# Kernel tuning notes

Hardware: AMD Instinct MI355X
Metric: run time of the kernel (lower is better)

The kernel has to match this reference:

```python
import jax, jax.numpy as jnp
import numpy as np

D_MODEL, D_INNER, D_STATE, NHEADS, HEADDIM, D_CONV, CHUNK = 1024, 2048, 128, 32, 64, 4, 64
B_SZ, L = 2, 2048
EPS = 1e-5


def _segsum_exp(x):
    # x: (..., T) -> exp of lower-triangular cumulative segment sums, (..., T, T)
    cs = jnp.cumsum(x, axis=-1)
    seg = cs[..., :, None] - cs[..., None, :]
    T = x.shape[-1]
    mask = jnp.tril(jnp.ones((T, T), dtype=bool))
    return jnp.exp(jnp.where(mask, seg, 0.0)) * mask


def ssd(x, A, B, C, chunk):
    # x: (b,l,h,p), A: (b,l,h), B,C: (b,l,n)
    b, l, h, p = x.shape
    n = B.shape[-1]
    c = l // chunk
    x = x.reshape(b, c, chunk, h, p)
    A = A.reshape(b, c, chunk, h).transpose(0, 3, 1, 2)        # (b,h,c,s)
    B = B.reshape(b, c, chunk, n)
    C = C.reshape(b, c, chunk, n)
    A_cum = jnp.cumsum(A, axis=-1)                              # (b,h,c,s)
    Lmat = _segsum_exp(A)                                       # (b,h,c,s,s)
    # intra-chunk (diagonal block) output
    Y_diag = jnp.einsum('bcln,bcsn,bhcls,bcshp->bclhp', C, B, Lmat, x)
    # per-chunk final states
    decay_states = jnp.exp(A_cum[..., -1:] - A_cum)             # (b,h,c,s)
    states = jnp.einsum('bcsn,bhcs,bcshp->bchpn', B, decay_states, x)
    states = jnp.concatenate([jnp.zeros_like(states[:, :1]), states], axis=1)  # (b,c+1,h,p,n)
    # inter-chunk recurrence over chunk sums
    chunk_sums = jnp.pad(A_cum[..., -1], ((0, 0), (0, 0), (1, 0)))  # (b,h,c+1)
    decay_chunk = _segsum_exp(chunk_sums)                       # (b,h,c+1,c+1)
    new_states = jnp.einsum('bhzc,bchpn->bzhpn', decay_chunk, states)
    states_in, final_state = new_states[:, :-1], new_states[:, -1]
    out_decay = jnp.exp(A_cum)                                  # (b,h,c,s)
    Y_off = jnp.einsum('bcln,bchpn,bhcl->bclhp', C, states_in, out_decay)
    Y = (Y_diag + Y_off).reshape(b, l, h, p)
    return Y, final_state


def causal_depthwise_conv(x, w, b):
    # x: (B, C, L), w: (C, K), b: (C,)
    K = w.shape[-1]
    Llen = x.shape[-1]
    xp = jnp.pad(x, ((0, 0), (0, 0), (K - 1, 0)))
    out = b[None, :, None]
    for k in range(K):
        out = out + w[None, :, k, None] * xp[:, :, k:k + Llen]
    return out


def setup_inputs() -> dict:
    key = jax.random.key(0)
    ks = jax.random.split(key, 9)
    d_in_proj = 2 * D_INNER + 2 * D_STATE + NHEADS
    conv_dim = D_INNER + 2 * D_STATE
    return {
        'u': jax.random.normal(ks[0], (B_SZ, L, D_MODEL), jnp.float32),
        'W_in': jax.random.normal(ks[1], (d_in_proj, D_MODEL), jnp.float32) * (D_MODEL ** -0.5),
        'conv_w': jax.random.normal(ks[2], (conv_dim, D_CONV), jnp.float32) * (D_CONV ** -0.5),
        'conv_b': jax.random.normal(ks[3], (conv_dim,), jnp.float32) * 0.01,
        'dt_bias': jax.random.normal(ks[4], (NHEADS,), jnp.float32),
        'A_log': jnp.log(1.0 + 15.0 * jax.random.uniform(ks[5], (NHEADS,), jnp.float32)),
        'D': jax.random.normal(ks[6], (NHEADS,), jnp.float32),
        'norm_w': jnp.ones((D_INNER,), jnp.float32),
        'W_out': jax.random.normal(ks[8], (D_MODEL, D_INNER), jnp.float32) * (D_INNER ** -0.5),
    }


def reference(u, W_in, conv_w, conv_b, dt_bias, A_log, D, norm_w, W_out):
    zxbcdt = u @ W_in.T                                        # (B,L,d_in_proj)
    z = zxbcdt[..., :D_INNER]
    xBC = zxbcdt[..., D_INNER:2 * D_INNER + 2 * D_STATE]
    dt = jax.nn.softplus(zxbcdt[..., -NHEADS:] + dt_bias)      # (B,L,H)
    # causal depthwise conv + silu
    xBC = causal_depthwise_conv(xBC.transpose(0, 2, 1), conv_w, conv_b).transpose(0, 2, 1)
    xBC = jax.nn.silu(xBC)
    A = -jnp.exp(A_log)                                        # (H,)
    x = xBC[..., :D_INNER].reshape(u.shape[0], u.shape[1], NHEADS, HEADDIM)
    Bm = xBC[..., D_INNER:D_INNER + D_STATE]
    Cm = xBC[..., D_INNER + D_STATE:]
    y, _ = ssd(x * dt[..., None], A * dt, Bm, Cm, CHUNK)
    y = y + x * D[:, None]
    y = y.reshape(u.shape[0], u.shape[1], D_INNER)
    # gated RMSNorm
    y = y * jax.nn.silu(z)
    y = y * jax.lax.rsqrt(jnp.mean(y * y, axis=-1, keepdims=True) + EPS) * norm_w
    return y @ W_out.T
```

## Files before the change

### kernel.cpp

```cpp
#include <hip/hip_runtime.h>
#include <hip/hip_bf16.h>
#include <math.h>

#define D_MODEL 1024
#define D_INNER 2048
#define D_STATE 128
#define NHEADS 32
#define HEADDIM 64
#define CHUNK 64
#define B_SZ 2
#define LSEQ 2048
#define BL (B_SZ*LSEQ)
#define DPROJ (2*D_INNER + 2*D_STATE + NHEADS)
#define CONV_DIM (D_INNER + 2*D_STATE)
#define NCHUNK (LSEQ/CHUNK)
#define NPAD1 4480
#define EPSF 1e-5f

typedef __attribute__((ext_vector_type(8))) _Float16 half8;
typedef __attribute__((ext_vector_type(4))) _Float16 half4;
typedef __attribute__((ext_vector_type(4))) float f32x4;

__device__ __forceinline__ float siluf(float v){ return v / (1.0f + expf(-v)); }
__device__ __forceinline__ float softplusf(float v){ return v > 20.0f ? v : log1pf(expf(v)); }
__device__ __forceinline__ unsigned short f2h(float x){
  union { _Float16 h; unsigned short u; } v; v.h = (_Float16)x;
  return v.u;
}
__device__ __forceinline__ float h2f(unsigned short x){
  union { unsigned short u; _Float16 h; } v; v.u = x;
  return (float)v.h;
}
__device__ __forceinline__ _Float16 h2h(unsigned short x){
  union { unsigned short u; _Float16 h; } v; v.u = x;
  return v.h;
}

typedef const __attribute__((address_space(1))) void gvoid_t;
typedef __attribute__((address_space(3))) void lvoid_t;
__device__ __forceinline__ void gl_lds16(const void* gsrc, void* ldst) {
  gvoid_t* g = reinterpret_cast<gvoid_t*>((uintptr_t)gsrc);
  lvoid_t* l = reinterpret_cast<lvoid_t*>((unsigned int)(uintptr_t)ldst);
  __builtin_amdgcn_global_load_lds(g, l, 16, 0, 0);
}

#define NU4  (BL*D_MODEL/4)
#define NW4  (NPAD1*D_MODEL/4)
#define NWo4 (D_MODEL*D_INNER/4)
#define NCVT (NU4+NW4+NWo4)

__global__ void cvt_all(const float* __restrict__ u, const float* __restrict__ W_in,
                        const float* __restrict__ W_out, const float* __restrict__ norm_w,
                        unsigned short* __restrict__ u_h, unsigned short* __restrict__ Win_h,
                        unsigned short* __restrict__ Wg_h) {
  int i = blockIdx.x*256 + threadIdx.x;
  if (i >= NCVT) return;
  if (i < NU4) {
    float4 v = *(const float4*)(u + (size_t)i*4);
    ushort4 o; o.x=f2h(v.x); o.y=f2h(v.y); o.z=f2h(v.z); o.w=f2h(v.w);
    *(ushort4*)(u_h + (size_t)i*4) = o;
  } else if (i < NU4 + NW4) {
    int q = i - NU4;
    int row = q / (D_MODEL/4);
    ushort4 o; o.x=0; o.y=0; o.z=0; o.w=0;
    if (row < DPROJ) {
      float4 v = *(const float4*)(W_in + (size_t)q*4);
      o.x=f2h(v.x); o.y=f2h(v.y); o.z=f2h(v.z); o.w=f2h(v.w);
    }
    *(ushort4*)(Win_h + (size_t)q*4) = o;
  } else {
    int q = i - NU4 - NW4;
    int colq = q % (D_INNER/4);
    float4 v = *(const float4*)(W_out + (size_t)q*4);
    float4 g = *(const float4*)(norm_w + (size_t)colq*4);
    ushort4 o; o.x=f2h(v.x*g.x); o.y=f2h(v.y*g.y); o.z=f2h(v.z*g.z); o.w=f2h(v.w*g.w);
    *(ushort4*)(Wg_h + (size_t)q*4) = o;
  }
}

template<int OUT_F16>
__global__ __launch_bounds__(256) void gemm_f16_pipe(const unsigned short* __restrict__ A,
    const unsigned short* __restrict__ W, void* __restrict__ Cv,
    const float* __restrict__ Sc, int N, int K) {
  __shared__ unsigned short lds[4*2*4096];
  const int t   = threadIdx.x;
  const int wid = t >> 6, l = t & 63;
  const int gx = gridDim.x, gy = gridDim.y;
  int bid = blockIdx.y * gx + blockIdx.x;
  int k   = bid & 7;
  int j   = bid >> 3;
  int rpx = gy >> 3;
  int r   = j % rpx;
  int colIdx = j / rpx;
  int row = k*rpx + r;
  int col = (colIdx + k*(gx >> 3)) % gx;
  const int m0 = row * 128;
  const int n0 = col * 128;
  const int wr = wid >> 1, wc = wid & 1;
  const int fr = l & 15, cg = l >> 4;
  const int NT = K >> 5;

  int srow[2]; int scol[2];
  #pragma unroll
  for (int i=0;i<2;++i){
    int s = i*256 + t;
    int rr = s >> 2, c = s & 3;
    int sw = (rr + (rr>>2)) & 3;
    srow[i] = rr; scol[i] = (c ^ sw) * 8;
  }
  const unsigned short* Abase = A + (size_t)m0 * K;
  const unsigned short* Wbase = W + (size_t)n0 * K;

#define STAGE(tt, slot) { \
    int kk = (tt) << 5; \
    unsigned short* La = &lds[(slot)*8192]; \
    unsigned short* Lb = &lds[(slot)*8192 + 4096]; \
    gl_lds16(Abase + (size_t)srow[0]*K + kk + scol[0], (char*)La + (0*256+t)*16); \
    gl_lds16(Abase + (size_t)srow[1]*K + kk + scol[1], (char*)La + (1*256+t)*16); \
    gl_lds16(Wbase + (size_t)srow[0]*K + kk + scol[0], (char*)Lb + (0*256+t)*16); \
    gl_lds16(Wbase + (size_t)srow[1]*K + kk + scol[1], (char*)Lb + (1*256+t)*16); \
  }

#define COMPUTE(slot) { \
    const unsigned short* La = &lds[(slot)*8192]; \
    const unsigned short* Lb = &lds[(slot)*8192 + 4096]; \
    half8 af[4], bfv[4]; \
    _Pragma("unroll") \
    for (int m=0;m<4;++m){ \
      int rr = wr*64 + m*16 + fr; \
      int sw = (rr + (rr>>2)) & 3; \
      af[m] = *(const half8*)&La[(rr*4 + (cg ^ sw))*8]; \
    } \
    _Pragma("unroll") \
    for (int n=0;n<4;++n){ \
      int rr = wc*64 + n*16 + fr; \
      int sw = (rr + (rr>>2)) & 3; \
      bfv[n] = *(const half8*)&Lb[(rr*4 + (cg ^ sw))*8]; \
    } \
    __builtin_amdgcn_s_setprio(1); \
    _Pragma("unroll") \
    for (int m=0;m<4;++m) \
      _Pragma("unroll") \
      for (int n=0;n<4;++n) \
        acc[m][n] = __builtin_amdgcn_mfma_f32_16x16x32_f16(af[m], bfv[n], acc[m][n], 0, 0, 0); \
    __builtin_amdgcn_s_setprio(0); \
  }

  f32x4 acc[4][4] = {};
  STAGE(0, 0);
  STAGE(1, 1);
  STAGE(2, 2);
  STAGE(3, 3);

  for (int tt = 0; tt < NT; tt += 2) {
    if (tt + 4 < NT) { asm volatile("s_waitcnt vmcnt(8)" ::: "memory"); }
    else             { asm volatile("s_waitcnt vmcnt(0)" ::: "memory"); }
    __builtin_amdgcn_s_barrier();
    asm volatile("" ::: "memory");

    COMPUTE(tt & 3);
    COMPUTE((tt + 1) & 3);

    asm volatile("s_waitcnt lgkmcnt(0)" ::: "memory");
    __builtin_amdgcn_s_barrier();
    asm volatile("" ::: "memory");
    if (tt + 4 < NT) {
      STAGE(tt + 4, (tt + 4) & 3);
      if (tt + 5 < NT) STAGE(tt + 5, (tt + 5) & 3);
    }
  }
#undef COMPUTE
#undef STAGE

  const int crow = m0 + wr*64 + (l >> 4) * 4;
  const int ccol0 = n0 + wc*64 + fr;
  #pragma unroll
  for (int m = 0; m < 4; ++m) {
    #pragma unroll
    for (int n = 0; n < 4; ++n) {
      int colo = ccol0 + n*16;
      if (colo < N) {
        if (OUT_F16) {
          unsigned short* cp = (unsigned short*)Cv + (size_t)(crow + m*16)*N + colo;
          #pragma unroll
          for (int jj = 0; jj < 4; ++jj) cp[(size_t)jj*N] = f2h(acc[m][n][jj]);
        } else {
          float* cp = (float*)Cv + (size_t)(crow + m*16)*N + colo;
          #pragma unroll
          for (int jj = 0; jj < 4; ++jj) cp[(size_t)jj*N] = acc[m][n][jj] * Sc[crow + m*16 + jj];
        }
      }
    }
  }
}

__global__ __launch_bounds__(256) void gemm_f16_64(const unsigned short* __restrict__ A,
    const unsigned short* __restrict__ W, float* __restrict__ C,
    const float* __restrict__ Sc, int N, int K) {
  __shared__ unsigned short lds[4*6144];
  const int t   = threadIdx.x;
  const int wid = t >> 6, l = t & 63;
  const int gx = gridDim.x, gy = gridDim.y;
  int bid = blockIdx.y * gx + blockIdx.x;
  int k   = bid & 7;
  int j   = bid >> 3;
  int rpx = gy >> 3;
  int r   = j % rpx;
  int colIdx = j / rpx;
  const int m0 = (k*rpx + r) * 64;
  const int n0 = ((colIdx + k*(gx >> 3)) % gx) * 128;
  const int fr = l & 15, cg = l >> 4;
  const int NT = K >> 5;

  const int srw  = t >> 2;
  const int sw_  = (srw + (srw>>2)) & 3;
  const int scl  = ((t & 3) ^ sw_) * 8;
  const unsigned short* Abase = A + (size_t)m0 * K;
  const unsigned short* Wbase = W + (size_t)n0 * K;

#define STG64(tt, slot) { \
    int kk = (tt) << 5; \
    char* Ls = (char*)lds + (slot)*12288; \
    gl_lds16(Abase + (size_t)srw*K + kk + scl,        Ls + t*16); \
    gl_lds16(Wbase + (size_t)srw*K + kk + scl,        Ls + 4096 + t*16); \
    gl_lds16(Wbase + (size_t)(64+srw)*K + kk + scl,   Ls + 4096 + (256+t)*16); \
  }

#define CMP64(slot) { \
    const unsigned short* La = &lds[(slot)*6144]; \
    const unsigned short* Lb = &lds[(slot)*6144 + 2048]; \
    half8 af[4], bfv[2]; \
    _Pragma("unroll") \
    for (int m=0;m<4;++m){ \
      int rr = m*16 + fr; \
      int sw = (rr + (rr>>2)) & 3; \
      af[m] = *(const half8*)&La[(rr*4 + (cg ^ sw))*8]; \
    } \
    _Pragma("unroll") \
    for (int n=0;n<2;++n){ \
      int rr = wid*32 + n*16 + fr; \
      int sw = (rr + (rr>>2)) & 3; \
      bfv[n] = *(const half8*)&Lb[(rr*4 + (cg ^ sw))*8]; \
    } \
    __builtin_amdgcn_s_setprio(1); \
    _Pragma("unroll") \
    for (int m=0;m<4;++m) \
      _Pragma("unroll") \
      for (int n=0;n<2;++n) \
        acc[m][n] = __builtin_amdgcn_mfma_f32_16x16x32_f16(af[m], bfv[n], acc[m][n], 0, 0, 0); \
    __builtin_amdgcn_s_setprio(0); \
  }

  f32x4 acc[4][2] = {};
  STG64(0, 0);
  STG64(1, 1);
  STG64(2, 2);
  STG64(3, 3);

  for (int tt = 0; tt < NT; tt += 2) {
    if (tt + 4 < NT) { asm volatile("s_waitcnt vmcnt(6)" ::: "memory"); }
    else             { asm volatile("s_waitcnt vmcnt(0)" ::: "memory"); }
    __builtin_amdgcn_s_barrier();
    asm volatile("" ::: "memory");

    CMP64(tt & 3);
    CMP64((tt + 1) & 3);

    asm volatile("s_waitcnt lgkmcnt(0)" ::: "memory");
    __builtin_amdgcn_s_barrier();
    asm volatile("" ::: "memory");
    if (tt + 4 < NT) {
      STG64(tt + 4, (tt + 4) & 3);
      if (tt + 5 < NT) STG64(tt + 5, (tt + 5) & 3);
    }
  }
#undef CMP64
#undef STG64

  const int crow = m0 + cg * 4;
  const int ccol0 = n0 + wid*32 + fr;
  #pragma unroll
  for (int m = 0; m < 4; ++m) {
    #pragma unroll
    for (int n = 0; n < 2; ++n) {
      int colo = ccol0 + n*16;
      float* cp = C + (size_t)(crow + m*16)*N + colo;
      #pragma unroll
      for (int jj = 0; jj < 4; ++jj) cp[(size_t)jj*N] = acc[m][n][jj] * Sc[crow + m*16 + jj];
    }
  }
}

__global__ __launch_bounds__(64) void dtacum_kernel(const unsigned short* __restrict__ zx,
    const float* __restrict__ dt_bias, const float* __restrict__ A_log,
    float* __restrict__ dt, float* __restrict__ A_cum) {
  int blk = blockIdx.x;
  int c = blk & 31, h = (blk >> 5) & 31, b = blk >> 10;
  int l = threadIdx.x;
  int row = b*LSEQ + c*CHUNK + l;
  float v = h2f(zx[(size_t)row*DPROJ + (2*D_INNER + 2*D_STATE) + h]) + dt_bias[h];
  float dtv = softplusf(v);
  dt[row*NHEADS + h] = dtv;
  float val = -expf(A_log[h]) * dtv;
  #pragma unroll
  for (int off = 1; off < 64; off <<= 1) {
    float nv = __shfl_up(val, off, 64);
    if (l >= off) val += nv;
  }
  A_cum[blk*64 + l] = val;
}

__global__ __launch_bounds__(256) void conv8_kernel(const unsigned short* __restrict__ zx,
    const float* __restrict__ w, const float* __restrict__ bias, unsigned short* __restrict__ xBC) {
  int idx = blockIdx.x*256 + threadIdx.x;
  if (idx >= (BL/8)*(CONV_DIM/4)) return;
  int c4  = idx % (CONV_DIM/4);
  int rb  = idx / (CONV_DIM/4);
  int ch  = c4 * 4;
  int row0 = rb * 8;
  int l0   = row0 & (LSEQ-1);
  float4 r[11];
  #pragma unroll
  for (int jj=0;jj<11;++jj){
    int li = l0 + jj - 3;
    if (li >= 0) {
      ushort4 v = *(const ushort4*)&zx[(size_t)(row0 + jj - 3)*DPROJ + D_INNER + ch];
      r[jj] = make_float4(h2f(v.x), h2f(v.y), h2f(v.z), h2f(v.w));
    } else r[jj] = make_float4(0.f,0.f,0.f,0.f);
  }
  float4 wv[4];
  #pragma unroll
  for (int c=0;c<4;++c) wv[c] = *(const float4*)&w[(ch+c)*4];
  float4 bv = *(const float4*)&bias[ch];
  #pragma unroll
  for (int j=0;j<8;++j){
    float4 acc = bv;
    acc.x += wv[0].x*r[j].x + wv[0].y*r[j+1].x + wv[0].z*r[j+2].x + wv[0].w*r[j+3].x;
    acc.y += wv[1].x*r[j].y + wv[1].y*r[j+1].y + wv[1].z*r[j+2].y + wv[1].w*r[j+3].y;
    acc.z += wv[2].x*r[j].z + wv[2].y*r[j+1].z + wv[2].z*r[j+2].z + wv[2].w*r[j+3].z;
    acc.w += wv[3].x*r[j].w + wv[3].y*r[j+1].w + wv[3].z*r[j+2].w + wv[3].w*r[j+3].w;
    ushort4 o; o.x=f2h(siluf(acc.x)); o.y=f2h(siluf(acc.y)); o.z=f2h(siluf(acc.z)); o.w=f2h(siluf(acc.w));
    *(ushort4*)&xBC[(size_t)(row0+j)*CONV_DIM + ch] = o;
  }
}

__global__ __launch_bounds__(256) void g_kernel(const unsigned short* __restrict__ xBC,
                                                unsigned short* __restrict__ G) {
  int blk = blockIdx.x >> 2;
  int lq  = blockIdx.x & 3;
  int b = blk >> 5, c = blk & 31;
  __shared__ float Bsh[64][129];
  int t = threadIdx.x;
  int row0 = b*LSEQ + c*CHUNK;
  #pragma unroll
  for (int j=0;j<8;++j){
    int e0 = (j*256 + t)*4;
    int s = e0 >> 7, n = e0 & 127;
    ushort4 v = *(const ushort4*)&xBC[(size_t)(row0+s)*CONV_DIM + D_INNER + n];
    Bsh[s][n+0] = h2f(v.x); Bsh[s][n+1] = h2f(v.y);
    Bsh[s][n+2] = h2f(v.z); Bsh[s][n+3] = h2f(v.w);
  }
  __syncthreads();
  int l = lq*16 + (t >> 4), s0 = (t & 15) * 4;
  const unsigned short* Cp = &xBC[(size_t)(row0+l)*CONV_DIM + D_INNER + D_STATE];
  float acc[4] = {};
  #pragma unroll 4
  for (int n4=0;n4<32;++n4){
    ushort4 cv4 = *(const ushort4*)&Cp[n4*4];
    float cv[4] = { h2f(cv4.x), h2f(cv4.y), h2f(cv4.z), h2f(cv4.w) };
    #pragma unroll
    for (int kk=0;kk<4;++kk){
      #pragma unroll
      for (int j=0;j<4;++j) acc[j] += cv[kk] * Bsh[s0+j][n4*4+kk];
    }
  }
  unsigned short* Gp = &G[(size_t)blk*4096 + l*64 + s0];
  ushort4 o; o.x=f2h(acc[0]); o.y=f2h(acc[1]); o.z=f2h(acc[2]); o.w=f2h(acc[3]);
  *(ushort4*)Gp = o;
}

__global__ __launch_bounds__(256) void states_mfma(const unsigned short* __restrict__ xBC,
    const float* __restrict__ dt, const float* __restrict__ A_cum, unsigned short* __restrict__ states) {
  int blk = blockIdx.x;
  int h = blk & 31, c = (blk>>5)&31, b = blk>>10;
  __shared__ _Float16 Bt[128][72];
  __shared__ _Float16 xdT[64][72];
  __shared__ float Ac[64], dtl[64];
  int t = threadIdx.x;
  int wid = t >> 6, ln = t & 63;
  int row0 = b*LSEQ + c*CHUNK;
  if (t < 64){ Ac[t] = A_cum[((b*32+h)*32 + c)*64 + t]; dtl[t] = dt[(row0+t)*NHEADS + h]; }
  __syncthreads();
  float AcL = Ac[63];
  #pragma unroll
  for (int j=0;j<8;++j){
    int e0 = (j*256+t)*4;
    int s = e0 >> 7, n = e0 & 127;
    ushort4 v = *(const ushort4*)&xBC[(size_t)(row0+s)*CONV_DIM + D_INNER + n];
    Bt[n+0][s] = h2h(v.x); Bt[n+1][s] = h2h(v.y);
    Bt[n+2][s] = h2h(v.z); Bt[n+3][s] = h2h(v.w);
  }
  #pragma unroll
  for (int j=0;j<4;++j){
    int e0 = (j*256+t)*4;
    int s = e0 >> 6, p = e0 & 63;
    float sc = dtl[s] * expf(AcL - Ac[s]);
    ushort4 v = *(const ushort4*)&xBC[(size_t)(row0+s)*CONV_DIM + h*HEADDIM + p];
    xdT[p+0][s] = (_Float16)(h2f(v.x)*sc);
    xdT[p+1][s] = (_Float16)(h2f(v.y)*sc);
    xdT[p+2][s] = (_Float16)(h2f(v.z)*sc);
    xdT[p+3][s] = (_Float16)(h2f(v.w)*sc);
  }
  __syncthreads();
  const int fr = ln & 15, fk = (ln >> 4) * 8;
  f32x4 acc[4][2] = {};
  #pragma unroll
  for (int ks = 0; ks < 2; ++ks){
    half8 a[4], bb[2];
    #pragma unroll
    for (int pt=0;pt<4;++pt) a[pt] = *(const half8*)&xdT[pt*16+fr][ks*32+fk];
    #pragma unroll
    for (int nt=0;nt<2;++nt) bb[nt] = *(const half8*)&Bt[(wid*2+nt)*16+fr][ks*32+fk];
    #pragma unroll
    for (int pt=0;pt<4;++pt)
      #pragma unroll
      for (int nt=0;nt<2;++nt)
        acc[pt][nt] = __builtin_amdgcn_mfma_f32_16x16x32_f16(a[pt], bb[nt], acc[pt][nt], 0, 0, 0);
  }
  unsigned short* Sp = &states[(size_t)blk*8192];
  #pragma unroll
  for (int pt=0;pt<4;++pt){
    int p0 = pt*16 + (ln>>4)*4;
    #pragma unroll
    for (int nt=0;nt<2;++nt){
      int n = (wid*2+nt)*16 + fr;
      #pragma unroll
      for (int j=0;j<4;++j) Sp[(p0+j)*128 + n] = f2h(acc[pt][nt][j]);
    }
  }
}

__global__ __launch_bounds__(256) void scan_kernel(const float* __restrict__ A_cum,
                                                   unsigned short* __restrict__ states) {
  int g  = blockIdx.x & 7;
  int bh = blockIdx.x >> 3;
  int b = bh >> 5, h = bh & 31;
  int t = threadIdx.x;
  int off = g*1024 + t*4;
  ushort4 tmp[NCHUNK];
  float dec[NCHUNK];
  #pragma unroll
  for (int c=0;c<NCHUNK;++c){
    tmp[c] = *(const ushort4*)&states[(size_t)((b*32+c)*32 + h)*8192 + off];
    dec[c] = A_cum[((b*32+h)*32 + c)*64 + 63];
  }
  float s0=0.f, s1=0.f, s2=0.f, s3=0.f;
  #pragma unroll
  for (int c=0;c<NCHUNK;++c){
    float d = expf(dec[c]);
    ushort4 o; o.x=f2h(s0); o.y=f2h(s1); o.z=f2h(s2); o.w=f2h(s3);
    *(ushort4*)&states[(size_t)((b*32+c)*32 + h)*8192 + off] = o;
    s0 = s0*d + h2f(tmp[c].x);
    s1 = s1*d + h2f(tmp[c].y);
    s2 = s2*d + h2f(tmp[c].z);
    s3 = s3*d + h2f(tmp[c].w);
  }
}

__global__ __launch_bounds__(256) void y_mfma(const unsigned short* __restrict__ xBC,
    const unsigned short* __restrict__ zx, const float* __restrict__ dt,
    const float* __restrict__ A_cum, const unsigned short* __restrict__ G,
    const unsigned short* __restrict__ states, const float* __restrict__ Dp,
    unsigned short* __restrict__ y_pre) {
  int blk = blockIdx.x;
  int h = blk & 31, c = (blk>>5)&31, b = blk>>10;
  __shared__ _Float16 Cl[64][136];
  __shared__ _Float16 Sin[64][136];
  __shared__ _Float16 Ms[64][72];
  __shared__ _Float16 xdT[64][72];
  __shared__ float Ac[64], dtl[64];
  int t = threadIdx.x;
  int wid = t >> 6, ln = t & 63;
  int row0 = b*LSEQ + c*CHUNK;
  if (t < 64){ Ac[t] = A_cum[((b*32+h)*32 + c)*64 + t]; dtl[t] = dt[(row0+t)*NHEADS + h]; }
  __syncthreads();
  #pragma unroll
  for (int j=0;j<8;++j){
    int e0 = (j*256+t)*4; int l = e0>>7, n = e0&127;
    float sc = expf(Ac[l]);
    ushort4 v = *(const ushort4*)&xBC[(size_t)(row0+l)*CONV_DIM + D_INNER + D_STATE + n];
    half4 hv = { (_Float16)(h2f(v.x)*sc), (_Float16)(h2f(v.y)*sc),
                 (_Float16)(h2f(v.z)*sc), (_Float16)(h2f(v.w)*sc) };
    *(half4*)&Cl[l][n] = hv;
  }
  {
    const unsigned short* Sg = &states[(size_t)blk*8192];
    #pragma unroll
    for (int j=0;j<8;++j){
      int elem = (j*256+t)*4; int p = elem>>7, n = elem&127;
      ushort4 v = *(const ushort4*)&Sg[elem];
      half4 hv = { h2h(v.x), h2h(v.y), h2h(v.z), h2h(v.w) };
      *(half4*)&Sin[p][n] = hv;
    }
  }
  #pragma unroll
  for (int j=0;j<4;++j){
    int e0 = (j*256+t)*4; int s = e0>>6, p = e0&63;
    float sc = dtl[s];
    ushort4 v = *(const ushort4*)&xBC[(size_t)(row0+s)*CONV_DIM + h*HEADDIM + p];
    xdT[p+0][s] = (_Float16)(h2f(v.x)*sc);
    xdT[p+1][s] = (_Float16)(h2f(v.y)*sc);
    xdT[p+2][s] = (_Float16)(h2f(v.z)*sc);
    xdT[p+3][s] = (_Float16)(h2f(v.w)*sc);
  }
  {
    const unsigned short* Gp = &G[(size_t)(b*32+c)*4096];
    #pragma unroll
    for (int j=0;j<4;++j){
      int e0 = (j*256+t)*4; int l = e0>>6, s = e0&63;
      ushort4 gv = *(const ushort4*)&Gp[e0];
      float al = Ac[l];
      Ms[l][s+0] = (s+0 <= l) ? (_Float16)(h2f(gv.x) * expf(al-Ac[s+0])) : (_Float16)0.f;
      Ms[l][s+1] = (s+1 <= l) ? (_Float16)(h2f(gv.y) * expf(al-Ac[s+1])) : (_Float16)0.f;
      Ms[l][s+2] = (s+2 <= l) ? (_Float16)(h2f(gv.z) * expf(al-Ac[s+2])) : (_Float16)0.f;
      Ms[l][s+3] = (s+3 <= l) ? (_Float16)(h2f(gv.w) * expf(al-Ac[s+3])) : (_Float16)0.f;
    }
  }
  __syncthreads();
  const int wr = wid >> 1, wc = wid & 1;
  const int fr = ln & 15, fk = (ln >> 4) * 8;
  f32x4 acc[2][2] = {};
  #pragma unroll
  for (int ks = 0; ks < 4; ++ks){
    half8 a[2], bb[2];
    #pragma unroll
    for (int lt=0;lt<2;++lt) a[lt] = *(const half8*)&Cl[(wr*2+lt)*16+fr][ks*32+fk];
    #pragma unroll
    for (int pt=0;pt<2;++pt) bb[pt] = *(const half8*)&Sin[(wc*2+pt)*16+fr][ks*32+fk];
    #pragma unroll
    for (int lt=0;lt<2;++lt)
      #pragma unroll
      for (int pt=0;pt<2;++pt)
        acc[lt][pt] = __builtin_amdgcn_mfma_f32_16x16x32_f16(a[lt], bb[pt], acc[lt][pt], 0, 0, 0);
  }
  #pragma unroll
  for (int ks = 0; ks < 2; ++ks){
    half8 a[2], bb[2];
    #pragma unroll
    for (int lt=0;lt<2;++lt) a[lt] = *(const half8*)&Ms[(wr*2+lt)*16+fr][ks*32+fk];
    #pragma unroll
    for (int pt=0;pt<2;++pt) bb[pt] = *(const half8*)&xdT[(wc*2+pt)*16+fr][ks*32+fk];
    #pragma unroll
    for (int lt=0;lt<2;++lt)
      #pragma unroll
      for (int pt=0;pt<2;++pt)
        acc[lt][pt] = __builtin_amdgcn_mfma_f32_16x16x32_f16(a[lt], bb[pt], acc[lt][pt], 0, 0, 0);
  }
  float Dh = Dp[h];
  #pragma unroll
  for (int lt=0;lt<2;++lt){
    int l0 = (wr*2+lt)*16 + (ln>>4)*4;
    #pragma unroll
    for (int pt=0;pt<2;++pt){
      int p = (wc*2+pt)*16 + fr;
      #pragma unroll
      for (int j=0;j<4;++j){
        int grow = row0 + l0 + j;
        float x = h2f(xBC[(size_t)grow*CONV_DIM + h*HEADDIM + p]);
        float z = h2f(zx[(size_t)grow*DPROJ + h*HEADDIM + p]);
        y_pre[(size_t)grow*D_INNER + h*HEADDIM + p] = f2h((acc[lt][pt][j] + x*Dh) * siluf(z));
      }
    }
  }
}

__global__ __launch_bounds__(256) void rowsc_kernel(const unsigned short* __restrict__ y,
                                                    float* __restrict__ sc) {
  int row = blockIdx.x;
  int t = threadIdx.x;
  const unsigned short* yr = y + (size_t)row*D_INNER + t*8;
  ushort4 a = *(const ushort4*)yr;
  ushort4 bq = *(const ushort4*)(yr+4);
  float ss = 0.f;
  float v;
  v=h2f(a.x); ss+=v*v; v=h2f(a.y); ss+=v*v; v=h2f(a.z); ss+=v*v; v=h2f(a.w); ss+=v*v;
  v=h2f(bq.x); ss+=v*v; v=h2f(bq.y); ss+=v*v; v=h2f(bq.z); ss+=v*v; v=h2f(bq.w); ss+=v*v;
  #pragma unroll
  for (int off=32; off>0; off>>=1) ss += __shfl_down(ss, off, 64);
  __shared__ float wsum[4];
  int wid = t >> 6, lane = t & 63;
  if (lane == 0) wsum[wid] = ss;
  __syncthreads();
  if (t == 0) sc[row] = rsqrtf((wsum[0]+wsum[1]+wsum[2]+wsum[3])/D_INNER + EPSF);
}

extern "C" void kernel_launch(void* const* d_in, const int* in_sizes, int n_in,
                              void* d_out, int out_size, void* d_ws, size_t ws_size,
                              hipStream_t stream) {
  const float* u       = (const float*)d_in[0];
  const float* W_in    = (const float*)d_in[1];
  const float* conv_w  = (const float*)d_in[2];
  const float* conv_b  = (const float*)d_in[3];
  const float* dt_bias = (const float*)d_in[4];
  const float* A_log   = (const float*)d_in[5];
  const float* Dp      = (const float*)d_in[6];
  const float* norm_w  = (const float*)d_in[7];
  const float* W_out   = (const float*)d_in[8];
  float* out = (float*)d_out;

  char* w = (char*)d_ws;
  unsigned short* zx_h   = (unsigned short*)w;  w += (size_t)BL*DPROJ*2;
  unsigned short* xBC_h  = (unsigned short*)w;  w += (size_t)BL*CONV_DIM*2;
  unsigned short* ypre_h = (unsigned short*)w;  w += (size_t)BL*D_INNER*2;
  unsigned short* u_h    = (unsigned short*)w;  w += (size_t)BL*D_MODEL*2;
  unsigned short* Win_h  = (unsigned short*)w;  w += (size_t)NPAD1*D_MODEL*2;
  unsigned short* Wg_h   = (unsigned short*)w;  w += (size_t)D_MODEL*D_INNER*2;
  unsigned short* states = (unsigned short*)w;  w += (size_t)B_SZ*NCHUNK*NHEADS*HEADDIM*D_STATE*2;
  unsigned short* G      = (unsigned short*)w;  w += (size_t)B_SZ*NCHUNK*CHUNK*CHUNK*2;
  float* dt     = (float*)w;  w += (size_t)BL*NHEADS*4;
  float* A_cum  = (float*)w;  w += (size_t)B_SZ*NHEADS*NCHUNK*CHUNK*4;
  float* sc     = (float*)w;  w += (size_t)BL*4;

  cvt_all<<<(NCVT+255)/256, 256, 0, stream>>>(u, W_in, W_out, norm_w, u_h, Win_h, Wg_h);
  gemm_f16_pipe<1><<<dim3(NPAD1/128, BL/128), 256, 0, stream>>>(u_h, Win_h, zx_h, nullptr, DPROJ, D_MODEL);
  dtacum_kernel<<<B_SZ*NHEADS*NCHUNK, 64, 0, stream>>>(zx_h, dt_bias, A_log, dt, A_cum);
  conv8_kernel<<<((BL/8)*(CONV_DIM/4)+255)/256, 256, 0, stream>>>(zx_h, conv_w, conv_b, xBC_h);
  g_kernel<<<B_SZ*NCHUNK*4, 256, 0, stream>>>(xBC_h, G);
  states_mfma<<<B_SZ*NCHUNK*NHEADS, 256, 0, stream>>>(xBC_h, dt, A_cum, states);
  scan_kernel<<<B_SZ*NHEADS*8, 256, 0, stream>>>(A_cum, states);
  y_mfma<<<B_SZ*NCHUNK*NHEADS, 256, 0, stream>>>(xBC_h, zx_h, dt, A_cum, G, states, Dp, ypre_h);
  rowsc_kernel<<<BL, 256, 0, stream>>>(ypre_h, sc);
  gemm_f16_64<<<dim3(D_MODEL/128, BL/64), 256, 0, stream>>>(ypre_h, Wg_h, out, sc, D_MODEL, D_INNER);
}
```

Before: 185.3 us.

## Fuse RMS sum-of-squares into y_mfma via atomics; conv processes 16 rows

Removes the separate row-scale kernel. y_mfma now computes per-row partial sums of squares and accumulates them with atomicAdd into a buffer that dtacum zeroes, and the output GEMM applies rsqrt in its epilogue. The conv kernel also handles 16 rows per thread instead of 8, reusing more of the loaded halo. This saves one launch and a full re-read of y_pre, at the cost of atomic contention (32 heads × 4 column groups per row) and non-deterministic fp32 summation. The sums are taken before fp16 rounding of y_pre.

Measured after the change: 197.1 us. 6.3% more time.

```diff
diff --git a/kernel.cpp b/kernel.cpp
--- a/kernel.cpp
+++ b/kernel.cpp
@@ -196,7 +196,7 @@
 
 __global__ __launch_bounds__(256) void gemm_f16_64(const unsigned short* __restrict__ A,
     const unsigned short* __restrict__ W, float* __restrict__ C,
-    const float* __restrict__ Sc, int N, int K) {
+    const float* __restrict__ ScRaw, int N, int K) {
   __shared__ unsigned short lds[4*6144];
   const int t   = threadIdx.x;
   const int wid = t >> 6, l = t & 63;
@@ -286,15 +286,19 @@
       int colo = ccol0 + n*16;
       float* cp = C + (size_t)(crow + m*16)*N + colo;
       #pragma unroll
-      for (int jj = 0; jj < 4; ++jj) cp[(size_t)jj*N] = acc[m][n][jj] * Sc[crow + m*16 + jj];
+      for (int jj = 0; jj < 4; ++jj) {
+        float scv = rsqrtf(ScRaw[crow + m*16 + jj] * (1.0f/D_INNER) + EPSF);
+        cp[(size_t)jj*N] = acc[m][n][jj] * scv;
+      }
     }
   }
 }
 
 __global__ __launch_bounds__(64) void dtacum_kernel(const unsigned short* __restrict__ zx,
     const float* __restrict__ dt_bias, const float* __restrict__ A_log,
-    float* __restrict__ dt, float* __restrict__ A_cum) {
+    float* __restrict__ dt, float* __restrict__ A_cum, float* __restrict__ sc_raw) {
   int blk = blockIdx.x;
+  if (blk < 64) sc_raw[blk*64 + threadIdx.x] = 0.f;
   int c = blk & 31, h = (blk >> 5) & 31, b = blk >> 10;
   int l = threadIdx.x;
   int row = b*LSEQ + c*CHUNK + l;
@@ -310,18 +314,18 @@
   A_cum[blk*64 + l] = val;
 }
 
-__global__ __launch_bounds__(256) void conv8_kernel(const unsigned short* __restrict__ zx,
+__global__ __launch_bounds__(256) void conv16_kernel(const unsigned short* __restrict__ zx,
     const float* __restrict__ w, const float* __restrict__ bias, unsigned short* __restrict__ xBC) {
   int idx = blockIdx.x*256 + threadIdx.x;
-  if (idx >= (BL/8)*(CONV_DIM/4)) return;
+  if (idx >= (BL/16)*(CONV_DIM/4)) return;
   int c4  = idx % (CONV_DIM/4);
   int rb  = idx / (CONV_DIM/4);
   int ch  = c4 * 4;
-  int row0 = rb * 8;
+  int row0 = rb * 16;
   int l0   = row0 & (LSEQ-1);
-  float4 r[11];
-  #pragma unroll
-  for (int jj=0;jj<11;++jj){
+  float4 r[19];
+  #pragma unroll
+  for (int jj=0;jj<19;++jj){
     int li = l0 + jj - 3;
     if (li >= 0) {
       ushort4 v = *(const ushort4*)&zx[(size_t)(row0 + jj - 3)*DPROJ + D_INNER + ch];
@@ -333,7 +337,7 @@
   for (int c=0;c<4;++c) wv[c] = *(const float4*)&w[(ch+c)*4];
   float4 bv = *(const float4*)&bias[ch];
   #pragma unroll
-  for (int j=0;j<8;++j){
+  for (int j=0;j<16;++j){
     float4 acc = bv;
     acc.x += wv[0].x*r[j].x + wv[0].y*r[j+1].x + wv[0].z*r[j+2].x + wv[0].w*r[j+3].x;
     acc.y += wv[1].x*r[j].y + wv[1].y*r[j+1].y + wv[1].z*r[j+2].y + wv[1].w*r[j+3].y;
@@ -471,7 +475,7 @@
     const unsigned short* __restrict__ zx, const float* __restrict__ dt,
     const float* __restrict__ A_cum, const unsigned short* __restrict__ G,
     const unsigned short* __restrict__ states, const float* __restrict__ Dp,
-    unsigned short* __restrict__ y_pre) {
+    unsigned short* __restrict__ y_pre, float* __restrict__ sc_raw) {
   int blk = blockIdx.x;
   int h = blk & 31, c = (blk>>5)&31, b = blk>>10;
   __shared__ _Float16 Cl[64][136];
@@ -561,37 +565,25 @@
   for (int lt=0;lt<2;++lt){
     int l0 = (wr*2+lt)*16 + (ln>>4)*4;
     #pragma unroll
-    for (int pt=0;pt<2;++pt){
-      int p = (wc*2+pt)*16 + fr;
+    for (int j=0;j<4;++j){
+      int grow = row0 + l0 + j;
+      float s = 0.f;
       #pragma unroll
-      for (int j=0;j<4;++j){
-        int grow = row0 + l0 + j;
+      for (int pt=0;pt<2;++pt){
+        int p = (wc*2+pt)*16 + fr;
         float x = h2f(xBC[(size_t)grow*CONV_DIM + h*HEADDIM + p]);
         float z = h2f(zx[(size_t)grow*DPROJ + h*HEADDIM + p]);
-        y_pre[(size_t)grow*D_INNER + h*HEADDIM + p] = f2h((acc[lt][pt][j] + x*Dh) * siluf(z));
+        float yv = (acc[lt][pt][j] + x*Dh) * siluf(z);
+        y_pre[(size_t)grow*D_INNER + h*HEADDIM + p] = f2h(yv);
+        s += yv*yv;
       }
-    }
-  }
-}
-
-__global__ __launch_bounds__(256) void rowsc_kernel(const unsigned short* __restrict__ y,
-                                                    float* __restrict__ sc) {
-  int row = blockIdx.x;
-  int t = threadIdx.x;
-  const unsigned short* yr = y + (size_t)row*D_INNER + t*8;
-  ushort4 a = *(const ushort4*)yr;
-  ushort4 bq = *(const ushort4*)(yr+4);
-  float ss = 0.f;
-  float v;
-  v=h2f(a.x); ss+=v*v; v=h2f(a.y); ss+=v*v; v=h2f(a.z); ss+=v*v; v=h2f(a.w); ss+=v*v;
-  v=h2f(bq.x); ss+=v*v; v=h2f(bq.y); ss+=v*v; v=h2f(bq.z); ss+=v*v; v=h2f(bq.w); ss+=v*v;
-  #pragma unroll
-  for (int off=32; off>0; off>>=1) ss += __shfl_down(ss, off, 64);
-  __shared__ float wsum[4];
-  int wid = t >> 6, lane = t & 63;
-  if (lane == 0) wsum[wid] = ss;
-  __syncthreads();
-  if (t == 0) sc[row] = rsqrtf((wsum[0]+wsum[1]+wsum[2]+wsum[3])/D_INNER + EPSF);
+      s += __shfl_xor(s, 1, 64);
+      s += __shfl_xor(s, 2, 64);
+      s += __shfl_xor(s, 4, 64);
+      s += __shfl_xor(s, 8, 64);
+      if (fr == 0) atomicAdd(&sc_raw[grow], s);
+    }
+  }
 }
 
 extern "C" void kernel_launch(void* const* d_in, const int* in_sizes, int n_in,
@@ -619,16 +611,15 @@
   unsigned short* G      = (unsigned short*)w;  w += (size_t)B_SZ*NCHUNK*CHUNK*CHUNK*2;
   float* dt     = (float*)w;  w += (size_t)BL*NHEADS*4;
   float* A_cum  = (float*)w;  w += (size_t)B_SZ*NHEADS*NCHUNK*CHUNK*4;
-  float* sc     = (float*)w;  w += (size_t)BL*4;
+  float* sc_raw = (float*)w;  w += (size_t)BL*4;
 
   cvt_all<<<(NCVT+255)/256, 256, 0, stream>>>(u, W_in, W_out, norm_w, u_h, Win_h, Wg_h);
   gemm_f16_pipe<1><<<dim3(NPAD1/128, BL/128), 256, 0, stream>>>(u_h, Win_h, zx_h, nullptr, DPROJ, D_MODEL);
-  dtacum_kernel<<<B_SZ*NHEADS*NCHUNK, 64, 0, stream>>>(zx_h, dt_bias, A_log, dt, A_cum);
-  conv8_kernel<<<((BL/8)*(CONV_DIM/4)+255)/256, 256, 0, stream>>>(zx_h, conv_w, conv_b, xBC_h);
+  dtacum_kernel<<<B_SZ*NHEADS*NCHUNK, 64, 0, stream>>>(zx_h, dt_bias, A_log, dt, A_cum, sc_raw);
+  conv16_kernel<<<((BL/16)*(CONV_DIM/4)+255)/256, 256, 0, stream>>>(zx_h, conv_w, conv_b, xBC_h);
   g_kernel<<<B_SZ*NCHUNK*4, 256, 0, stream>>>(xBC_h, G);
   states_mfma<<<B_SZ*NCHUNK*NHEADS, 256, 0, stream>>>(xBC_h, dt, A_cum, states);
   scan_kernel<<<B_SZ*NHEADS*8, 256, 0, stream>>>(A_cum, states);
-  y_mfma<<<B_SZ*NCHUNK*NHEADS, 256, 0, stream>>>(xBC_h, zx_h, dt, A_cum, G, states, Dp, ypre_h);
-  rowsc_kernel<<<BL, 256, 0, stream>>>(ypre_h, sc);
-  gemm_f16_64<<<dim3(D_MODEL/128, BL/64), 256, 0, stream>>>(ypre_h, Wg_h, out, sc, D_MODEL, D_INNER);
-}
+  y_mfma<<<B_SZ*NCHUNK*NHEADS, 256, 0, stream>>>(xBC_h, zx_h, dt, A_cum, G, states, Dp, ypre_h, sc_raw);
+  gemm_f16_64<<<dim3(D_MODEL/128, BL/64), 256, 0, stream>>>(ypre_h, Wg_h, out, sc_raw, D_MODEL, D_INNER);
+}
```
